# Performance work log

Measured on AMD Instinct MI355X. Metric: run time of the kernel, lower is better.

Reference implementation:

```python
import jax, jax.numpy as jnp
import numpy as np

N, E, D, B = 50000, 800000, 64, 64
NEXP, NC, EDIM, PDIM = 4, 10, 4, 100


def setup_inputs() -> dict:
    key = jax.random.key(0)
    ks = jax.random.split(key, 24)
    s = lambda f: 1.0 / np.sqrt(f)
    inp = {
        'x': jax.random.normal(ks[0], (N, D), jnp.float32),
        'edge_index': jax.random.randint(ks[1], (2, E), 0, N, jnp.int32),
        'edge_attr': jax.random.normal(ks[2], (E, EDIM), jnp.float32),
        'batch': jnp.sort(jax.random.randint(ks[3], (N,), 0, B, jnp.int32)),
        'ldxb_flag': jax.random.normal(ks[4], (B,), jnp.float32),
        # layer 1 params
        'w_edge1': jax.random.normal(ks[5], (D, EDIM)) * s(EDIM),
        'b_edge1': jnp.zeros((D,), jnp.float32),
        'w_ih1': jax.random.normal(ks[6], (3 * D, D)) * s(D),
        'w_hh1': jax.random.normal(ks[7], (3 * D, D)) * s(D),
        'b_ih1': jnp.zeros((3 * D,), jnp.float32),
        'b_hh1': jnp.zeros((3 * D,), jnp.float32),
        # layer 2 params
        'w_edge2': jax.random.normal(ks[8], (D, EDIM)) * s(EDIM),
        'b_edge2': jnp.zeros((D,), jnp.float32),
        'w_ih2': jax.random.normal(ks[9], (3 * D, D)) * s(D),
        'w_hh2': jax.random.normal(ks[10], (3 * D, D)) * s(D),
        'b_ih2': jnp.zeros((3 * D,), jnp.float32),
        'b_hh2': jnp.zeros((3 * D,), jnp.float32),
        # MoE
        'gate_w': jax.random.normal(ks[11], (NEXP, D)) * s(D),
        'gate_b': jnp.zeros((NEXP,), jnp.float32),
        'exp_w': jax.random.normal(ks[12], (NEXP, D, D)) * s(D),
        'exp_b': jnp.zeros((NEXP, D), jnp.float32),
        # heads
        'proj_w': jax.random.normal(ks[13], (PDIM, 1)),
        'proj_b': jnp.zeros((PDIM,), jnp.float32),
        'fc_w': jax.random.normal(ks[14], (NC, D + PDIM)) * s(D + PDIM),
        'fc_b': jnp.zeros((NC,), jnp.float32),
    }
    return inp


def _ggnn_layer(x, src, dst, eemb, w_ih, w_hh, b_ih, b_hh):
    # gather + scatter-add message passing (self-loops already in src/dst/eemb)
    msg = x[src] + eemb                       # [E+N, D]
    m = jnp.zeros_like(x).at[dst].add(msg)    # [N, D]
    # GRUCell(m, x): x is the hidden state
    gi = m @ w_ih.T + b_ih
    gh = x @ w_hh.T + b_hh
    i_r, i_z, i_n = jnp.split(gi, 3, axis=1)
    h_r, h_z, h_n = jnp.split(gh, 3, axis=1)
    r = jax.nn.sigmoid(i_r + h_r)
    z = jax.nn.sigmoid(i_z + h_z)
    n = jnp.tanh(i_n + r * h_n)
    return (1.0 - z) * n + z * x


def reference(x, edge_index, edge_attr, batch, ldxb_flag,
              w_edge1, b_edge1, w_ih1, w_hh1, b_ih1, b_hh1,
              w_edge2, b_edge2, w_ih2, w_hh2, b_ih2, b_hh2,
              gate_w, gate_b, exp_w, exp_b, proj_w, proj_b, fc_w, fc_b):
    n = x.shape[0]
    loop = jnp.arange(n, dtype=edge_index.dtype)
    src = jnp.concatenate([edge_index[0], loop])
    dst = jnp.concatenate([edge_index[1], loop])
    ea = jnp.concatenate([edge_attr, jnp.zeros((n, edge_attr.shape[1]), edge_attr.dtype)], axis=0)

    h = _ggnn_layer(x, src, dst, ea @ w_edge1.T + b_edge1, w_ih1, w_hh1, b_ih1, b_hh1)
    h = jax.nn.relu(h)
    h = _ggnn_layer(h, src, dst, ea @ w_edge2.T + b_edge2, w_ih2, w_hh2, b_ih2, b_hh2)
    h = jax.nn.relu(h)

    # soft MoE combine
    gw = jax.nn.softmax(h @ gate_w.T + gate_b, axis=1)            # [N, NEXP]
    eo = jax.nn.relu(jnp.einsum('nd,ehd->neh', h, exp_w) + exp_b)  # [N, NEXP, D]
    h = jnp.einsum('ne,neh->nh', gw, eo)                           # [N, D]

    # global mean pool per graph
    sums = jax.ops.segment_sum(h, batch, num_segments=B)
    cnts = jax.ops.segment_sum(jnp.ones((n,), h.dtype), batch, num_segments=B)
    graph_emb = sums / jnp.maximum(cnts, 1.0)[:, None]             # [B, D]

    flag = ldxb_flag[:, None] @ proj_w.T + proj_b                  # [B, 100]
    logits = jnp.concatenate([flag, graph_emb], axis=1) @ fc_w.T + fc_b
    return (graph_emb, graph_emb, logits)
```

## Files before the change

kernel.cpp:

```cpp
#include <hip/hip_runtime.h>
#include <stdint.h>


#define SUBCAP 8
#define OVF_MAX 32768
#define PS 16

typedef __bf16 bf16x8 __attribute__((ext_vector_type(8)));
typedef float floatx4 __attribute__((ext_vector_type(4)));
typedef unsigned short us8 __attribute__((ext_vector_type(8)));

__device__ __forceinline__ unsigned short f2bf(float f){
  union { float f; unsigned u; } c; c.f = f;
  unsigned r = c.u + 0x7FFFu + ((c.u >> 16) & 1u);
  return (unsigned short)(r >> 16);
}
__device__ __forceinline__ float sigm(float x){ return 1.f/(1.f + __expf(-x)); }

__global__ void k_init(const float* __restrict__ s0, const float* __restrict__ s1,
                       const float* __restrict__ s2, const float* __restrict__ s3,
                       const float* __restrict__ s4, const float* __restrict__ s5,
                       unsigned short* __restrict__ dst,
                       int* __restrict__ cur, int* __restrict__ ovfcnt, int N8){
  int i = blockIdx.x*blockDim.x + threadIdx.x;
  if (i < N8) cur[i] = 0;
  if (i == 0){ ovfcnt[0] = 0; }
  if (i >= 65792) return;
  const float* s; int off;
  if      (i < 12288){ s = s0; off = i; }
  else if (i < 24576){ s = s1; off = i - 12288; }
  else if (i < 36864){ s = s2; off = i - 24576; }
  else if (i < 49152){ s = s3; off = i - 36864; }
  else if (i < 49408){ s = s4; off = i - 49152; }
  else               { s = s5; off = i - 49408; }
  dst[i] = f2bf(s[off]);
}

__global__ void k_bucket(const int* __restrict__ ei,
                         int* __restrict__ cur, int2* __restrict__ bkt,
                         int* __restrict__ ovfcnt, int* __restrict__ ovf, int E){
  int e = blockIdx.x*blockDim.x + threadIdx.x;
  if (e >= E) return;
  int sub = blockIdx.x & 7;
  int s = ei[e];
  int d = ei[E + e];
  int pos = atomicAdd(&cur[d*8 + sub], 1);
  if (pos < SUBCAP){
    bkt[(size_t)d*64 + sub*SUBCAP + pos] = make_int2(s, e);
  } else {
    int o = atomicAdd(ovfcnt, 1);
    if (o < OVF_MAX) ovf[o] = e;
  }
}

__global__ void __launch_bounds__(256) k_gather(
    const int* __restrict__ cur, const int2* __restrict__ bkt,
    const float* __restrict__ ea,
    const float* __restrict__ xin,
    const float* __restrict__ w_edge, const float* __restrict__ b_edge,
    float* __restrict__ m, int N){
  int n = (int)(((long long)blockIdx.x*blockDim.x + threadIdx.x) >> 6);
  if (n >= N) return;
  int d = threadIdx.x & 63;
  const int4* cp = (const int4*)(cur + (size_t)n*8);
  int4 c0 = cp[0], c1 = cp[1];
  int cnt0 = c0.x, cnt1 = c0.y, cnt2 = c0.z, cnt3 = c0.w;
  int cnt4 = c1.x, cnt5 = c1.y, cnt6 = c1.z, cnt7 = c1.w;
  int degAll = cnt0+cnt1+cnt2+cnt3+cnt4+cnt5+cnt6+cnt7;
  int cc[8];
  cc[0]=min(cnt0,SUBCAP); cc[1]=min(cnt1,SUBCAP); cc[2]=min(cnt2,SUBCAP); cc[3]=min(cnt3,SUBCAP);
  cc[4]=min(cnt4,SUBCAP); cc[5]=min(cnt5,SUBCAP); cc[6]=min(cnt6,SUBCAP); cc[7]=min(cnt7,SUBCAP);

  float4 wv = *(const float4*)(w_edge + d*4);
  float acc = xin[(size_t)n*64 + d] + (float)(degAll + 1) * b_edge[d];
  float esx = 0.f, esy = 0.f, esz = 0.f, esw = 0.f;

  int2 se = make_int2(0, -1);
  if ((d & 7) < cc[d >> 3]) se = bkt[(size_t)n*64 + d];
  if (se.y >= 0){
    float4 v = *(const float4*)(ea + (size_t)se.y*4);
    esx = v.x; esy = v.y; esz = v.z; esw = v.w;
  }
#pragma unroll
  for (int j = 0; j < 8; ++j){
    int cj = cc[j];
    for (int k = 0; k < cj; ++k){
      int s = __shfl(se.x, j*SUBCAP + k);
      acc += xin[(size_t)s*64 + d];
    }
  }
#pragma unroll
  for (int off = 1; off < 64; off <<= 1){
    esx += __shfl_xor(esx, off);
    esy += __shfl_xor(esy, off);
    esz += __shfl_xor(esz, off);
    esw += __shfl_xor(esw, off);
  }
  acc += esx*wv.x + esy*wv.y + esz*wv.z + esw*wv.w;
  m[(size_t)n*64 + d] = acc;
}

__global__ void k_ovf(const int* __restrict__ ei, const float* __restrict__ ea,
                      const float* __restrict__ xin, const float* __restrict__ w_edge,
                      const int* __restrict__ ovf, const int* __restrict__ ovfcnt,
                      float* __restrict__ m, int E){
  int cnt = *ovfcnt; if (cnt > OVF_MAX) cnt = OVF_MAX;
  int nwaves = (gridDim.x * blockDim.x) >> 6;
  int wid = (int)((blockIdx.x*blockDim.x + threadIdx.x) >> 6);
  int d = threadIdx.x & 63;
  for (int k = wid; k < cnt; k += nwaves){
    int e = ovf[k];
    int s = ei[e], dst = ei[E + e];
    float4 v  = *(const float4*)(ea + (size_t)e*4);
    float4 wv = *(const float4*)(w_edge + d*4);
    float msg = xin[(size_t)s*64 + d] + v.x*wv.x + v.y*wv.y + v.z*wv.z + v.w*wv.w;
    atomicAdd(&m[(size_t)dst*64 + d], msg);
  }
}

__global__ void __launch_bounds__(256) k_gru(
    const float* __restrict__ m, const float* x,
    const unsigned short* __restrict__ wih, const unsigned short* __restrict__ whh,
    const float* __restrict__ b_ih, const float* __restrict__ b_hh,
    float* out, int tiles, int N){
  int wid = (int)(((long long)blockIdx.x*blockDim.x + threadIdx.x) >> 6);
  if (wid >= tiles) return;
  int lane = threadIdx.x & 63;
  int col = lane & 15, quad = lane >> 4;
  int na = wid*16 + col; if (na > N-1) na = N-1;

  bf16x8 am[2], ax[2];
#pragma unroll
  for (int ks = 0; ks < 2; ++ks){
    int kb = ks*32 + quad*8;
    const float4* mp = (const float4*)(m + (size_t)na*64 + kb);
    float4 lo = mp[0], hi = mp[1];
    us8 tm;
    tm[0]=f2bf(lo.x); tm[1]=f2bf(lo.y); tm[2]=f2bf(lo.z); tm[3]=f2bf(lo.w);
    tm[4]=f2bf(hi.x); tm[5]=f2bf(hi.y); tm[6]=f2bf(hi.z); tm[7]=f2bf(hi.w);
    am[ks] = __builtin_bit_cast(bf16x8, tm);
    const float4* xp = (const float4*)(x + (size_t)na*64 + kb);
    float4 xlo = xp[0], xhi = xp[1];
    us8 tx;
    tx[0]=f2bf(xlo.x); tx[1]=f2bf(xlo.y); tx[2]=f2bf(xlo.z); tx[3]=f2bf(xlo.w);
    tx[4]=f2bf(xhi.x); tx[5]=f2bf(xhi.y); tx[6]=f2bf(xhi.z); tx[7]=f2bf(xhi.w);
    ax[ks] = __builtin_bit_cast(bf16x8, tx);
  }

  floatx4 ai[12], ah[12];
#pragma unroll
  for (int nt = 0; nt < 12; ++nt){ ai[nt] = (floatx4)0.f; ah[nt] = (floatx4)0.f; }
#pragma unroll
  for (int nt = 0; nt < 12; ++nt){
    int r = nt*16 + col;
#pragma unroll
    for (int ks = 0; ks < 2; ++ks){
      int kb = ks*32 + quad*8;
      bf16x8 bi = __builtin_bit_cast(bf16x8, *(const us8*)(wih + (size_t)r*64 + kb));
      ai[nt] = __builtin_amdgcn_mfma_f32_16x16x32_bf16(am[ks], bi, ai[nt], 0,0,0);
      bf16x8 bh = __builtin_bit_cast(bf16x8, *(const us8*)(whh + (size_t)r*64 + kb));
      ah[nt] = __builtin_amdgcn_mfma_f32_16x16x32_bf16(ax[ks], bh, ah[nt], 0,0,0);
    }
  }

#pragma unroll
  for (int nt = 0; nt < 4; ++nt){
    int d = nt*16 + col;
    float bir = b_ih[d],      bhr = b_hh[d];
    float biz = b_ih[64+d],   bhz = b_hh[64+d];
    float bin = b_ih[128+d],  bhn = b_hh[128+d];
#pragma unroll
    for (int rg = 0; rg < 4; ++rg){
      int node = wid*16 + quad*4 + rg;
      if (node >= N) continue;
      float rr = sigm(ai[nt  ][rg] + bir + ah[nt  ][rg] + bhr);
      float zz = sigm(ai[nt+4][rg] + biz + ah[nt+4][rg] + bhz);
      float nn = tanhf(ai[nt+8][rg] + bin + rr*(ah[nt+8][rg] + bhn));
      float xv = x[(size_t)node*64 + d];
      float hv = (1.f - zz)*nn + zz*xv;
      out[(size_t)node*64 + d] = fmaxf(hv, 0.f);
    }
  }
}

__global__ void __launch_bounds__(256) k_moe(
    const float* __restrict__ h,
    const unsigned short* __restrict__ gate_w, const float* __restrict__ gate_b,
    const unsigned short* __restrict__ exp_w,  const float* __restrict__ exp_b,
    float* __restrict__ v_out, int tiles, int N){
  __shared__ float gsm[4][16][4];
  int gwid = (int)(((long long)blockIdx.x*blockDim.x + threadIdx.x) >> 6);
  int w = threadIdx.x >> 6;
  int lane = threadIdx.x & 63;
  int col = lane & 15, quad = lane >> 4;
  bool active = gwid < tiles;

  floatx4 accg = (floatx4)0.f;
  floatx4 acce[4][4];
#pragma unroll
  for (int e=0;e<4;++e)
#pragma unroll
    for (int nt=0;nt<4;++nt) acce[e][nt] = (floatx4)0.f;

  if (active){
    int na = gwid*16 + col; if (na > N-1) na = N-1;
    bf16x8 a[2];
#pragma unroll
    for (int ks=0; ks<2; ++ks){
      int kb = ks*32 + quad*8;
      const float4* hp = (const float4*)(h + (size_t)na*64 + kb);
      float4 lo = hp[0], hi = hp[1];
      us8 th;
      th[0]=f2bf(lo.x); th[1]=f2bf(lo.y); th[2]=f2bf(lo.z); th[3]=f2bf(lo.w);
      th[4]=f2bf(hi.x); th[5]=f2bf(hi.y); th[6]=f2bf(hi.z); th[7]=f2bf(hi.w);
      a[ks] = __builtin_bit_cast(bf16x8, th);
      us8 braw = {0,0,0,0,0,0,0,0};
      if (col < 4) braw = *(const us8*)(gate_w + col*64 + kb);
      accg = __builtin_amdgcn_mfma_f32_16x16x32_bf16(a[ks], __builtin_bit_cast(bf16x8, braw), accg, 0,0,0);
    }
#pragma unroll
    for (int e=0;e<4;++e)
#pragma unroll
      for (int nt=0;nt<4;++nt)
#pragma unroll
        for (int ks=0;ks<2;++ks){
          int kb = ks*32 + quad*8;
          bf16x8 b = __builtin_bit_cast(bf16x8,
              *(const us8*)(exp_w + ((size_t)e*64 + nt*16 + col)*64 + kb));
          acce[e][nt] = __builtin_amdgcn_mfma_f32_16x16x32_bf16(a[ks], b, acce[e][nt], 0,0,0);
        }
    if (col < 4){
      float gb = gate_b[col];
#pragma unroll
      for (int rg=0;rg<4;++rg) gsm[w][quad*4+rg][col] = accg[rg] + gb;
    }
  }
  __syncthreads();
  if (!active) return;

#pragma unroll
  for (int rg=0; rg<4; ++rg){
    int nrow = quad*4 + rg;
    int node = gwid*16 + nrow;
    if (node >= N) continue;
    float g0=gsm[w][nrow][0], g1=gsm[w][nrow][1], g2=gsm[w][nrow][2], g3=gsm[w][nrow][3];
    float mx = fmaxf(fmaxf(g0,g1), fmaxf(g2,g3));
    float e0=__expf(g0-mx), e1=__expf(g1-mx), e2=__expf(g2-mx), e3=__expf(g3-mx);
    float inv = 1.f/(e0+e1+e2+e3);
    float w0=e0*inv, w1=e1*inv, w2=e2*inv, w3=e3*inv;
#pragma unroll
    for (int nt=0;nt<4;++nt){
      int o = nt*16 + col;
      float v = w0*fmaxf(acce[0][nt][rg] + exp_b[      o], 0.f)
              + w1*fmaxf(acce[1][nt][rg] + exp_b[ 64 + o], 0.f)
              + w2*fmaxf(acce[2][nt][rg] + exp_b[128 + o], 0.f)
              + w3*fmaxf(acce[3][nt][rg] + exp_b[192 + o], 0.f);
      v_out[(size_t)node*64 + o] = v;
    }
  }
}

__device__ __forceinline__ int lower_bound_i(const int* __restrict__ a, int n, int key){
  int lo = 0, hi = n;
  while (lo < hi){ int mid = (lo + hi) >> 1; if (a[mid] < key) lo = mid + 1; else hi = mid; }
  return lo;
}

__global__ void __launch_bounds__(256) k_pool(
    const float* __restrict__ v, const int* __restrict__ batch, int N,
    float* __restrict__ partial){
  __shared__ float red[4][64];
  int g = blockIdx.x / PS, s = blockIdx.x % PS;
  int t = threadIdx.x, d = t & 63, r = t >> 6;
  int start = lower_bound_i(batch, N, g);
  int end   = lower_bound_i(batch, N, g + 1);
  int len = end - start;
  int per = (len + PS - 1) / PS;
  int s0 = start + s*per;
  int s1 = s0 + per; if (s1 > end) s1 = end;
  float acc = 0.f;
  for (int i = s0 + r; i < s1; i += 4)
    acc += v[(size_t)i*64 + d];
  red[r][d] = acc;
  __syncthreads();
  if (r == 0)
    partial[(size_t)blockIdx.x*64 + d] = red[0][d] + red[1][d] + red[2][d] + red[3][d];
}

__global__ void __launch_bounds__(64) k_head(
    const float* __restrict__ partial, const int* __restrict__ batch, int N, int B,
    const float* __restrict__ ldxb,
    const float* __restrict__ proj_w, const float* __restrict__ proj_b,
    const float* __restrict__ fc_w, const float* __restrict__ fc_b,
    float* __restrict__ out){
  __shared__ float ges[64];
  int b = blockIdx.x, d = threadIdx.x;
  int start = lower_bound_i(batch, N, b);
  int end   = lower_bound_i(batch, N, b + 1);
  float sum = 0.f;
#pragma unroll
  for (int s = 0; s < PS; ++s)
    sum += partial[((size_t)b*PS + s)*64 + d];
  float ge = sum / fmaxf((float)(end - start), 1.f);
  ges[d] = ge;
  out[(size_t)b*64 + d]                = ge;
  out[(size_t)B*64 + (size_t)b*64 + d] = ge;
  __syncthreads();
  if (d < 10){
    float acc = fc_b[d];
    float fl = ldxb[b];
    const float* fr = fc_w + d*164;
    for (int p = 0; p < 100; ++p) acc += (fl*proj_w[p] + proj_b[p]) * fr[p];
    for (int dd = 0; dd < 64; ++dd) acc += ges[dd]*fr[100 + dd];
    out[(size_t)B*128 + (size_t)b*10 + d] = acc;
  }
}

extern "C" void kernel_launch(void* const* d_in, const int* in_sizes, int n_in,
                              void* d_out, int out_size, void* d_ws, size_t ws_size,
                              hipStream_t stream){
  const float* x      = (const float*)d_in[0];
  const int*   ei     = (const int*)d_in[1];
  const float* ea     = (const float*)d_in[2];
  const int*   batch  = (const int*)d_in[3];
  const float* ldxb   = (const float*)d_in[4];
  const float* w_edge1= (const float*)d_in[5];
  const float* b_edge1= (const float*)d_in[6];
  const float* w_ih1  = (const float*)d_in[7];
  const float* w_hh1  = (const float*)d_in[8];
  const float* b_ih1  = (const float*)d_in[9];
  const float* b_hh1  = (const float*)d_in[10];
  const float* w_edge2= (const float*)d_in[11];
  const float* b_edge2= (const float*)d_in[12];
  const float* w_ih2  = (const float*)d_in[13];
  const float* w_hh2  = (const float*)d_in[14];
  const float* b_ih2  = (const float*)d_in[15];
  const float* b_hh2  = (const float*)d_in[16];
  const float* gate_w = (const float*)d_in[17];
  const float* gate_b = (const float*)d_in[18];
  const float* exp_w  = (const float*)d_in[19];
  const float* exp_b  = (const float*)d_in[20];
  const float* proj_w = (const float*)d_in[21];
  const float* proj_b = (const float*)d_in[22];
  const float* fc_w   = (const float*)d_in[23];
  const float* fc_b   = (const float*)d_in[24];
  float* out = (float*)d_out;

  int N = in_sizes[0] / 64;
  int E = in_sizes[1] / 2;
  int B = in_sizes[4];
  int tiles = (N + 15) / 16;
  int nTot = N * 64;

  float* m      = (float*)d_ws;
  float* h      = m + (size_t)nTot;
  int2*  bkt    = (int2*)(h + (size_t)nTot);
  int*   cur    = (int*)(bkt + (size_t)N*64);
  int*   ovfcnt = cur + (size_t)N*8;
  int*   ovf    = ovfcnt + 4;
  unsigned short* wbf = (unsigned short*)(ovf + OVF_MAX);
  float* partial = (float*)(wbf + 65792);
  unsigned short* wih1bf = wbf;
  unsigned short* whh1bf = wbf + 12288;
  unsigned short* wih2bf = wbf + 24576;
  unsigned short* whh2bf = wbf + 36864;
  unsigned short* gatebf = wbf + 49152;
  unsigned short* expbf  = wbf + 49408;

  dim3 blk(256);
  int edgeBlocks = (E + 255)/256;
  int nodeWaveBlocks = (N + 3)/4;
  int waveBlocks = (tiles + 3)/4;
  int N8 = N*8;
  int initBlocks = ((N8 > 65792 ? N8 : 65792) + 255)/256;

  k_init<<<initBlocks, blk, 0, stream>>>(w_ih1, w_hh1, w_ih2, w_hh2, gate_w, exp_w,
                                         wbf, cur, ovfcnt, N8);
  k_bucket<<<edgeBlocks, blk, 0, stream>>>(ei, cur, bkt, ovfcnt, ovf, E);
  k_gather<<<nodeWaveBlocks, blk, 0, stream>>>(cur, bkt, ea, x, w_edge1, b_edge1, m, N);
  k_ovf<<<8, blk, 0, stream>>>(ei, ea, x, w_edge1, ovf, ovfcnt, m, E);
  k_gru<<<waveBlocks, blk, 0, stream>>>(m, x, wih1bf, whh1bf, b_ih1, b_hh1, h, tiles, N);
  k_gather<<<nodeWaveBlocks, blk, 0, stream>>>(cur, bkt, ea, h, w_edge2, b_edge2, m, N);
  k_ovf<<<8, blk, 0, stream>>>(ei, ea, h, w_edge2, ovf, ovfcnt, m, E);
  k_gru<<<waveBlocks, blk, 0, stream>>>(m, h, wih2bf, whh2bf, b_ih2, b_hh2, h, tiles, N);
  k_moe<<<waveBlocks, blk, 0, stream>>>(h, gatebf, gate_b, expbf, exp_b, m, tiles, N);
  k_pool<<<B*PS, blk, 0, stream>>>(m, batch, N, partial);
  k_head<<<B, 64, 0, stream>>>(partial, batch, N, B, ldxb, proj_w, proj_b, fc_w, fc_b, out);
}
```

Measured before the change: 410.9 us.

## Split edge buckets into SoA src and bf16 edge-attr arrays, ballot-driven gather

The bucketing kernel now stores source indices and bf16-packed edge attributes in separate sub-bucket-major arrays, so the gather no longer does a dependent random load of edge_attr by edge id. The gather kernel reads one count per lane and reduces the degree with shuffles. It then walks valid neighbors via a ballot mask, issuing up to four independent row loads per iteration to raise memory-level parallelism. Edge attributes are rounded to bf16, which adds a small precision loss. The bucket kernel also does extra strided writes and an extra edge_attr read.

Result: faster. 365.6 us (-11.0%).

```diff
diff --git a/kernel.cpp b/kernel.cpp
--- a/kernel.cpp
+++ b/kernel.cpp
@@ -14,6 +14,9 @@
   union { float f; unsigned u; } c; c.f = f;
   unsigned r = c.u + 0x7FFFu + ((c.u >> 16) & 1u);
   return (unsigned short)(r >> 16);
+}
+__device__ __forceinline__ float bf2f(unsigned short u){
+  union { unsigned u; float f; } c; c.u = ((unsigned)u) << 16; return c.f;
 }
 __device__ __forceinline__ float sigm(float x){ return 1.f/(1.f + __expf(-x)); }
 
@@ -36,17 +39,23 @@
   dst[i] = f2bf(s[off]);
 }
 
-__global__ void k_bucket(const int* __restrict__ ei,
-                         int* __restrict__ cur, int2* __restrict__ bkt,
-                         int* __restrict__ ovfcnt, int* __restrict__ ovf, int E){
+__global__ void k_bucket(const int* __restrict__ ei, const float* __restrict__ ea,
+                         int* __restrict__ cur, int* __restrict__ bkt_src,
+                         ushort4* __restrict__ bkt_ea,
+                         int* __restrict__ ovfcnt, int* __restrict__ ovf,
+                         int E, int N){
   int e = blockIdx.x*blockDim.x + threadIdx.x;
   if (e >= E) return;
   int sub = blockIdx.x & 7;
   int s = ei[e];
   int d = ei[E + e];
-  int pos = atomicAdd(&cur[d*8 + sub], 1);
+  size_t sb = (size_t)sub*N + d;
+  int pos = atomicAdd(&cur[sb], 1);
   if (pos < SUBCAP){
-    bkt[(size_t)d*64 + sub*SUBCAP + pos] = make_int2(s, e);
+    float4 v = *(const float4*)(ea + (size_t)e*4);
+    ushort4 p; p.x = f2bf(v.x); p.y = f2bf(v.y); p.z = f2bf(v.z); p.w = f2bf(v.w);
+    bkt_src[sb*SUBCAP + pos] = s;
+    bkt_ea [sb*SUBCAP + pos] = p;
   } else {
     int o = atomicAdd(ovfcnt, 1);
     if (o < OVF_MAX) ovf[o] = e;
@@ -54,41 +63,58 @@
 }
 
 __global__ void __launch_bounds__(256) k_gather(
-    const int* __restrict__ cur, const int2* __restrict__ bkt,
-    const float* __restrict__ ea,
+    const int* __restrict__ cur, const int* __restrict__ bkt_src,
+    const ushort4* __restrict__ bkt_ea,
     const float* __restrict__ xin,
     const float* __restrict__ w_edge, const float* __restrict__ b_edge,
     float* __restrict__ m, int N){
   int n = (int)(((long long)blockIdx.x*blockDim.x + threadIdx.x) >> 6);
   if (n >= N) return;
   int d = threadIdx.x & 63;
-  const int4* cp = (const int4*)(cur + (size_t)n*8);
-  int4 c0 = cp[0], c1 = cp[1];
-  int cnt0 = c0.x, cnt1 = c0.y, cnt2 = c0.z, cnt3 = c0.w;
-  int cnt4 = c1.x, cnt5 = c1.y, cnt6 = c1.z, cnt7 = c1.w;
-  int degAll = cnt0+cnt1+cnt2+cnt3+cnt4+cnt5+cnt6+cnt7;
-  int cc[8];
-  cc[0]=min(cnt0,SUBCAP); cc[1]=min(cnt1,SUBCAP); cc[2]=min(cnt2,SUBCAP); cc[3]=min(cnt3,SUBCAP);
-  cc[4]=min(cnt4,SUBCAP); cc[5]=min(cnt5,SUBCAP); cc[6]=min(cnt6,SUBCAP); cc[7]=min(cnt7,SUBCAP);
+  int sub = d >> 3, k = d & 7;
+  size_t sb = (size_t)sub*N + n;
+  int myc = cur[sb];
+  int contrib = (k == 0) ? myc : 0;
+#pragma unroll
+  for (int off = 1; off < 64; off <<= 1) contrib += __shfl_xor(contrib, off);
+  int degAll = contrib;
+
+  bool valid = k < min(myc, SUBCAP);
+  int src = 0;
+  float esx = 0.f, esy = 0.f, esz = 0.f, esw = 0.f;
+  if (valid){
+    src = bkt_src[sb*SUBCAP + k];
+    ushort4 p = bkt_ea[sb*SUBCAP + k];
+    esx = bf2f(p.x); esy = bf2f(p.y); esz = bf2f(p.z); esw = bf2f(p.w);
+  }
 
   float4 wv = *(const float4*)(w_edge + d*4);
   float acc = xin[(size_t)n*64 + d] + (float)(degAll + 1) * b_edge[d];
-  float esx = 0.f, esy = 0.f, esz = 0.f, esw = 0.f;
-
-  int2 se = make_int2(0, -1);
-  if ((d & 7) < cc[d >> 3]) se = bkt[(size_t)n*64 + d];
-  if (se.y >= 0){
-    float4 v = *(const float4*)(ea + (size_t)se.y*4);
-    esx = v.x; esy = v.y; esz = v.z; esw = v.w;
-  }
-#pragma unroll
-  for (int j = 0; j < 8; ++j){
-    int cj = cc[j];
-    for (int k = 0; k < cj; ++k){
-      int s = __shfl(se.x, j*SUBCAP + k);
-      acc += xin[(size_t)s*64 + d];
-    }
-  }
+
+  unsigned long long mm = __ballot(valid);
+  while (mm){
+    int l0 = (int)__builtin_ctzll(mm); mm &= mm - 1;
+    int s0 = __shfl(src, l0);
+    float a0 = xin[(size_t)s0*64 + d];
+    float a1 = 0.f, a2 = 0.f, a3 = 0.f;
+    if (mm){
+      int l1 = (int)__builtin_ctzll(mm); mm &= mm - 1;
+      int s1 = __shfl(src, l1);
+      a1 = xin[(size_t)s1*64 + d];
+      if (mm){
+        int l2 = (int)__builtin_ctzll(mm); mm &= mm - 1;
+        int s2 = __shfl(src, l2);
+        a2 = xin[(size_t)s2*64 + d];
+        if (mm){
+          int l3 = (int)__builtin_ctzll(mm); mm &= mm - 1;
+          int s3 = __shfl(src, l3);
+          a3 = xin[(size_t)s3*64 + d];
+        }
+      }
+    }
+    acc += (a0 + a1) + (a2 + a3);
+  }
+
 #pragma unroll
   for (int off = 1; off < 64; off <<= 1){
     esx += __shfl_xor(esx, off);
@@ -352,14 +378,15 @@
   int tiles = (N + 15) / 16;
   int nTot = N * 64;
 
-  float* m      = (float*)d_ws;
-  float* h      = m + (size_t)nTot;
-  int2*  bkt    = (int2*)(h + (size_t)nTot);
-  int*   cur    = (int*)(bkt + (size_t)N*64);
-  int*   ovfcnt = cur + (size_t)N*8;
-  int*   ovf    = ovfcnt + 4;
+  float*   m       = (float*)d_ws;
+  float*   h       = m + (size_t)nTot;
+  int*     bkt_src = (int*)(h + (size_t)nTot);
+  ushort4* bkt_ea  = (ushort4*)(bkt_src + (size_t)nTot);
+  int*     cur     = (int*)(bkt_ea + (size_t)nTot);
+  int*     ovfcnt  = cur + (size_t)N*8;
+  int*     ovf     = ovfcnt + 4;
   unsigned short* wbf = (unsigned short*)(ovf + OVF_MAX);
-  float* partial = (float*)(wbf + 65792);
+  float*   partial = (float*)(wbf + 65792);
   unsigned short* wih1bf = wbf;
   unsigned short* whh1bf = wbf + 12288;
   unsigned short* wih2bf = wbf + 24576;
@@ -376,11 +403,11 @@
 
   k_init<<<initBlocks, blk, 0, stream>>>(w_ih1, w_hh1, w_ih2, w_hh2, gate_w, exp_w,
                                          wbf, cur, ovfcnt, N8);
-  k_bucket<<<edgeBlocks, blk, 0, stream>>>(ei, cur, bkt, ovfcnt, ovf, E);
-  k_gather<<<nodeWaveBlocks, blk, 0, stream>>>(cur, bkt, ea, x, w_edge1, b_edge1, m, N);
+  k_bucket<<<edgeBlocks, blk, 0, stream>>>(ei, ea, cur, bkt_src, bkt_ea, ovfcnt, ovf, E, N);
+  k_gather<<<nodeWaveBlocks, blk, 0, stream>>>(cur, bkt_src, bkt_ea, x, w_edge1, b_edge1, m, N);
   k_ovf<<<8, blk, 0, stream>>>(ei, ea, x, w_edge1, ovf, ovfcnt, m, E);
   k_gru<<<waveBlocks, blk, 0, stream>>>(m, x, wih1bf, whh1bf, b_ih1, b_hh1, h, tiles, N);
-  k_gather<<<nodeWaveBlocks, blk, 0, stream>>>(cur, bkt, ea, h, w_edge2, b_edge2, m, N);
+  k_gather<<<nodeWaveBlocks, blk, 0, stream>>>(cur, bkt_src, bkt_ea, h, w_edge2, b_edge2, m, N);
   k_ovf<<<8, blk, 0, stream>>>(ei, ea, h, w_edge2, ovf, ovfcnt, m, E);
   k_gru<<<waveBlocks, blk, 0, stream>>>(m, h, wih2bf, whh2bf, b_ih2, b_hh2, h, tiles, N);
   k_moe<<<waveBlocks, blk, 0, stream>>>(h, gatebf, gate_b, expbf, exp_b, m, tiles, N);
```
